# Performance work log

Measured on AMD Instinct MI355X. Metric: run time of the kernel, lower is better.

## Reference

```python
import jax, jax.numpy as jnp
import numpy as np

N_NODES = 50000
N_EDGES = 800000
X_DIM, H_DIM, Y_DIM = 128, 256, 128


def spmm(adj_vals, adj_row, adj_col, x):
    # sparse [N,N] @ dense [N,D] via gather + segment scatter-add
    msgs = adj_vals[:, None] * x[adj_col]  # [E, D]
    return jax.ops.segment_sum(msgs, adj_row, num_segments=N_NODES)


def setup_inputs() -> dict:
    key = jax.random.key(0)
    ks = jax.random.split(key, 6)
    x = jax.random.uniform(ks[0], (N_NODES, X_DIM), dtype=jnp.float32)
    adj_vals = jax.random.uniform(ks[1], (N_EDGES,), dtype=jnp.float32)
    adj_row = jax.random.randint(ks[2], (N_EDGES,), 0, N_NODES, dtype=jnp.int32)
    adj_col = jax.random.randint(ks[3], (N_EDGES,), 0, N_NODES, dtype=jnp.int32)
    W1 = jax.random.normal(ks[4], (X_DIM, H_DIM), dtype=jnp.float32) * (1.0 / np.sqrt(X_DIM))
    b1 = jnp.zeros((H_DIM,), dtype=jnp.float32)
    W2 = jax.random.normal(ks[5], (H_DIM, Y_DIM), dtype=jnp.float32) * (1.0 / np.sqrt(H_DIM))
    b2 = jnp.zeros((Y_DIM,), dtype=jnp.float32)
    return {"x": x, "adj_vals": adj_vals, "adj_row": adj_row, "adj_col": adj_col,
            "W1": W1, "b1": b1, "W2": W2, "b2": b2}


def reference(x, adj_vals, adj_row, adj_col, W1, b1, W2, b2):
    # row-normalize features: x / (sum_j x_ij + 1e-4)
    x = x / (jnp.sum(x, axis=1, keepdims=True) + 1e-4)
    # layer 1: spmm -> linear -> relu (dropout is identity at eval)
    h = jax.nn.relu(spmm(adj_vals, adj_row, adj_col, x) @ W1 + b1)  # [N, H]
    # layer 2: spmm -> linear
    y = spmm(adj_vals, adj_row, adj_col, h) @ W2 + b2  # [N, Y]
    return y
```

## Files before the change

### kernel.cpp

```cpp
#include <hip/hip_runtime.h>

#define N_NODES 50000
#define N_EDGES 800000
#define X_DIM 128
#define H_DIM 256
#define Y_DIM 128

typedef unsigned int uint32;
typedef unsigned short ushort16;
typedef __attribute__((ext_vector_type(8))) short short8;
typedef __attribute__((ext_vector_type(4))) float floatx4;

__device__ inline ushort16 f2bf(float f) {
    uint32 u = __float_as_uint(f);
    return (ushort16)((u + 0x7FFFu + ((u >> 16) & 1u)) >> 16);
}
__device__ inline float bf_lo(uint32 u) { return __uint_as_float(u << 16); }
__device__ inline float bf_hi(uint32 u) { return __uint_as_float(u & 0xFFFF0000u); }

#define BUCKET_SHIFT 7
#define NB 391
#define CHUNK 4096
#define NCHUNK 196
#define CAP_B 2560

#define NORM_BLOCKS 12500
#define CONV_BLOCKS 256

__global__ __launch_bounds__(256) void prep_kernel(
    const float* __restrict__ x, uint32* __restrict__ xb,
    const float* __restrict__ W1, const float* __restrict__ W2,
    ushort16* __restrict__ W1t, ushort16* __restrict__ W2t,
    const int* __restrict__ rows, int* __restrict__ gpartial) {
    int b = blockIdx.x;
    if (b < NORM_BLOCKS) {
        int row = (b * 256 + threadIdx.x) >> 6;
        int lane = threadIdx.x & 63;
        float2 v = ((const float2*)x)[(size_t)row * 64 + lane];
        float s = v.x + v.y;
        #pragma unroll
        for (int off = 32; off > 0; off >>= 1) s += __shfl_xor(s, off, 64);
        float inv = 1.0f / (s + 1e-4f);
        uint32 lo = (uint32)f2bf(v.x * inv);
        uint32 hi = (uint32)f2bf(v.y * inv);
        xb[(size_t)row * 64 + lane] = lo | (hi << 16);
    } else if (b < NORM_BLOCKS + CONV_BLOCKS) {
        int t = (b - NORM_BLOCKS) * 256 + threadIdx.x;
        if (t < X_DIM * H_DIM) {
            int n = t >> 7, k = t & 127;
            W1t[t] = f2bf(W1[k * H_DIM + n]);
        } else {
            int u = t - X_DIM * H_DIM;
            int y = u >> 8, k = u & 255;
            W2t[u] = f2bf(W2[k * Y_DIM + y]);
        }
    } else {
        __shared__ int h[NB];
        int j = b - NORM_BLOCKS - CONV_BLOCKS;
        int t = threadIdx.x;
        for (int i = t; i < NB; i += 256) h[i] = 0;
        __syncthreads();
        int base = j * CHUNK;
        #pragma unroll
        for (int k = 0; k < CHUNK / 256; k++) {
            int e = base + t + k * 256;
            if (e < N_EDGES) atomicAdd(&h[rows[e] >> BUCKET_SHIFT], 1);
        }
        __syncthreads();
        for (int i = t; i < NB; i += 256) gpartial[j * NB + i] = h[i];
    }
}

__global__ __launch_bounds__(512) void bucket_scan_kernel(
    const int* __restrict__ gpartial, int* __restrict__ bucket_base,
    int* __restrict__ bcursor, int* __restrict__ rowptr) {
    __shared__ int s[512];
    int t = threadIdx.x;
    int total = 0;
    if (t < NB) {
        #pragma unroll 4
        for (int j = 0; j < NCHUNK; j++) total += gpartial[j * NB + t];
    }
    s[t] = total;
    __syncthreads();
    #pragma unroll
    for (int off = 1; off < 512; off <<= 1) {
        int u = (t >= off) ? s[t - off] : 0;
        __syncthreads();
        s[t] += u;
        __syncthreads();
    }
    if (t < NB) {
        int excl = s[t] - total;
        bucket_base[t] = excl;
        bcursor[t] = excl;
    }
    if (t == 0) { bucket_base[NB] = N_EDGES; rowptr[N_NODES] = N_EDGES; }
}

__global__ __launch_bounds__(512) void bucketize_kernel(
    const int* __restrict__ rows, const int* __restrict__ cols,
    const float* __restrict__ vals, const int* __restrict__ gpartial,
    int* __restrict__ bcursor, int2* __restrict__ edges) {
    __shared__ int ob[512];
    __shared__ int c[NB];
    __shared__ int g[NB];
    __shared__ int2 buf[CHUNK];
    int t = threadIdx.x;
    int j = blockIdx.x;
    int base = j * CHUNK;
    int M = N_EDGES - base; if (M > CHUNK) M = CHUNK;
    int cnt = (t < NB) ? gpartial[j * NB + t] : 0;
    ob[t] = cnt;
    __syncthreads();
    #pragma unroll
    for (int off = 1; off < 512; off <<= 1) {
        int u = (t >= off) ? ob[t - off] : 0;
        __syncthreads();
        ob[t] += u;
        __syncthreads();
    }
    ob[t] -= cnt;
    if (t < NB) {
        c[t] = 0;
        g[t] = (cnt > 0) ? atomicAdd(&bcursor[t], cnt) : 0;
    }
    __syncthreads();
    #pragma unroll
    for (int k = 0; k < CHUNK / 512; k++) {
        int e = base + t + k * 512;
        if (e < N_EDGES) {
            int r = rows[e];
            int bb = r >> BUCKET_SHIFT;
            int p = ob[bb] + atomicAdd(&c[bb], 1);
            buf[p] = make_int2(cols[e] | ((r & 127) << 16) | (bb << 23),
                               __float_as_int(vals[e]));
        }
    }
    __syncthreads();
    for (int i = t; i < M; i += 512) {
        int2 e = buf[i];
        int bb = (int)((uint32)e.x >> 23);
        edges[g[bb] + (i - ob[bb])] = e;
    }
}

__global__ __launch_bounds__(256) void bucket_sort_kernel(
    const int* __restrict__ bucket_base, int2* __restrict__ edges,
    int2* __restrict__ scratch, int* __restrict__ rowptr) {
    __shared__ int2 buf[CAP_B];
    __shared__ int2 buf2[CAP_B];
    __shared__ int h[128], o[128], c[128];
    int b = blockIdx.x, t = threadIdx.x;
    int base = bucket_base[b];
    int cnt = bucket_base[b + 1] - base;
    bool fits = (cnt <= CAP_B);
    if (t < 128) h[t] = 0;
    __syncthreads();
    for (int i = t; i < cnt; i += 256) {
        int2 e = edges[base + i];
        if (fits) buf[i] = e; else scratch[base + i] = e;
        atomicAdd(&h[(e.x >> 16) & 127], 1);
    }
    __syncthreads();
    int valh = (t < 128) ? h[t] : 0;
    #pragma unroll
    for (int off = 1; off < 128; off <<= 1) {
        int u = (t >= off && t < 128) ? h[t - off] : 0;
        __syncthreads();
        if (t < 128) h[t] += u;
        __syncthreads();
    }
    if (t < 128) {
        o[t] = h[t] - valh;
        c[t] = 0;
        int i = (b << BUCKET_SHIFT) + t;
        if (i < N_NODES) rowptr[i] = base + h[t] - valh;
    }
    __syncthreads();
    for (int i = t; i < cnt; i += 256) {
        int2 e = fits ? buf[i] : scratch[base + i];
        int lr = (e.x >> 16) & 127;
        int p = o[lr] + atomicAdd(&c[lr], 1);
        if (fits) buf2[p] = e; else edges[base + p] = e;
    }
    __syncthreads();
    if (fits)
        for (int i = t; i < cnt; i += 256) edges[base + i] = buf2[i];
}

__device__ inline void spmm_row2(const uint2* __restrict__ feat2,
                                 const int2* __restrict__ edges,
                                 int start, int end, int lane,
                                 float& A0, float& A1, float& A2, float& A3) {
    const int hl = lane & 31;
    const int bsrc = lane & 32;
    float x0 = 0.f, x1 = 0.f, x2 = 0.f, x3 = 0.f;
    int cur = start;
    while (__any(cur < end)) {
        int n = end - cur;
        n = n < 0 ? 0 : (n > 32 ? 32 : n);
        int2 ev = make_int2(0, 0);
        if (hl < n) ev = edges[cur + hl];
        int c = ev.x & 0xFFFF;
        float v = __int_as_float(ev.y);
        int na = __shfl(n, 0, 64), nb = __shfl(n, 32, 64);
        int nm = na > nb ? na : nb;
        int jm = (nm + 7) & ~7;
        for (int j = 0; j < jm; j += 8) {
            int c0 = __shfl(c, bsrc + j, 64),     c1 = __shfl(c, bsrc + j + 1, 64);
            int c2 = __shfl(c, bsrc + j + 2, 64), c3 = __shfl(c, bsrc + j + 3, 64);
            int c4 = __shfl(c, bsrc + j + 4, 64), c5 = __shfl(c, bsrc + j + 5, 64);
            int c6 = __shfl(c, bsrc + j + 6, 64), c7 = __shfl(c, bsrc + j + 7, 64);
            float v0 = __shfl(v, bsrc + j, 64),     v1 = __shfl(v, bsrc + j + 1, 64);
            float v2 = __shfl(v, bsrc + j + 2, 64), v3 = __shfl(v, bsrc + j + 3, 64);
            float v4 = __shfl(v, bsrc + j + 4, 64), v5 = __shfl(v, bsrc + j + 5, 64);
            float v6 = __shfl(v, bsrc + j + 6, 64), v7 = __shfl(v, bsrc + j + 7, 64);
            uint2 f0 = feat2[(size_t)c0 * 32 + hl];
            uint2 f1 = feat2[(size_t)c1 * 32 + hl];
            uint2 f2 = feat2[(size_t)c2 * 32 + hl];
            uint2 f3 = feat2[(size_t)c3 * 32 + hl];
            uint2 f4 = feat2[(size_t)c4 * 32 + hl];
            uint2 f5 = feat2[(size_t)c5 * 32 + hl];
            uint2 f6 = feat2[(size_t)c6 * 32 + hl];
            uint2 f7 = feat2[(size_t)c7 * 32 + hl];
            x0 += v0 * bf_lo(f0.x); x1 += v0 * bf_hi(f0.x);
            x2 += v0 * bf_lo(f0.y); x3 += v0 * bf_hi(f0.y);
            x0 += v1 * bf_lo(f1.x); x1 += v1 * bf_hi(f1.x);
            x2 += v1 * bf_lo(f1.y); x3 += v1 * bf_hi(f1.y);
            x0 += v2 * bf_lo(f2.x); x1 += v2 * bf_hi(f2.x);
            x2 += v2 * bf_lo(f2.y); x3 += v2 * bf_hi(f2.y);
            x0 += v3 * bf_lo(f3.x); x1 += v3 * bf_hi(f3.x);
            x2 += v3 * bf_lo(f3.y); x3 += v3 * bf_hi(f3.y);
            x0 += v4 * bf_lo(f4.x); x1 += v4 * bf_hi(f4.x);
            x2 += v4 * bf_lo(f4.y); x3 += v4 * bf_hi(f4.y);
            x0 += v5 * bf_lo(f5.x); x1 += v5 * bf_hi(f5.x);
            x2 += v5 * bf_lo(f5.y); x3 += v5 * bf_hi(f5.y);
            x0 += v6 * bf_lo(f6.x); x1 += v6 * bf_hi(f6.x);
            x2 += v6 * bf_lo(f6.y); x3 += v6 * bf_hi(f6.y);
            x0 += v7 * bf_lo(f7.x); x1 += v7 * bf_hi(f7.x);
            x2 += v7 * bf_lo(f7.y); x3 += v7 * bf_hi(f7.y);
        }
        cur += n;
    }
    A0 = x0; A1 = x1; A2 = x2; A3 = x3;
}

__global__ __launch_bounds__(512, 4) void spmm_gemm_fused(
    const uint32* __restrict__ xb, const int* __restrict__ rowptr,
    const int2* __restrict__ edges, const ushort16* __restrict__ W1t,
    const ushort16* __restrict__ W2t, const float* __restrict__ b1,
    ushort16* __restrict__ hw) {
    __shared__ ushort16 a_s[64 * 136];
    __shared__ ushort16 h_s[64 * 264];
    const int tx = threadIdx.x;
    const int wave = tx >> 6, lane = tx & 63;
    const int quad = lane >> 4, l16 = lane & 15;
    const int half = lane >> 5, hl = lane & 31;
    const int row0 = blockIdx.x * 64;
    const uint2* xb2 = (const uint2*)xb;

    for (int i = 0; i < 4; i++) {
        int r = wave * 8 + i * 2 + half;
        int row = row0 + r;
        int s = 0, e = 0;
        if (row < N_NODES) { s = rowptr[row]; e = rowptr[row + 1]; }
        float a0, a1, a2, a3;
        spmm_row2(xb2, edges, s, e, lane, a0, a1, a2, a3);
        uint32 lo = (uint32)f2bf(a0) | ((uint32)f2bf(a1) << 16);
        uint32 hi = (uint32)f2bf(a2) | ((uint32)f2bf(a3) << 16);
        *(uint2*)&a_s[r * 136 + hl * 4] = make_uint2(lo, hi);
    }

    short8 bfr1[2][4];
    #pragma unroll
    for (int ct = 0; ct < 2; ct++)
        #pragma unroll
        for (int kk = 0; kk < 4; kk++)
            bfr1[ct][kk] = *(const short8*)
                &W1t[(wave * 32 + ct * 16 + l16) * 128 + kk * 32 + quad * 8];
    __syncthreads();

    floatx4 acc1[4][2];
    #pragma unroll
    for (int rs = 0; rs < 4; rs++)
        #pragma unroll
        for (int ct = 0; ct < 2; ct++)
            #pragma unroll
            for (int j = 0; j < 4; j++) acc1[rs][ct][j] = 0.f;
    #pragma unroll
    for (int kk = 0; kk < 4; kk++) {
        #pragma unroll
        for (int rs = 0; rs < 4; rs++) {
            short8 af = *(const short8*)&a_s[(rs * 16 + l16) * 136 + kk * 32 + quad * 8];
            #pragma unroll
            for (int ct = 0; ct < 2; ct++)
                acc1[rs][ct] = __builtin_amdgcn_mfma_f32_16x16x32_bf16(
                    af, bfr1[ct][kk], acc1[rs][ct], 0, 0, 0);
        }
    }
    float bv[2];
    #pragma unroll
    for (int ct = 0; ct < 2; ct++) bv[ct] = b1[wave * 32 + ct * 16 + l16];
    #pragma unroll
    for (int rs = 0; rs < 4; rs++)
        #pragma unroll
        for (int ct = 0; ct < 2; ct++)
            #pragma unroll
            for (int reg = 0; reg < 4; reg++) {
                float v = acc1[rs][ct][reg] + bv[ct];
                v = v > 0.f ? v : 0.f;
                h_s[(rs * 16 + quad * 4 + reg) * 264 + wave * 32 + ct * 16 + l16] = f2bf(v);
            }

    short8 bfr2[8];
    #pragma unroll
    for (int kk = 0; kk < 8; kk++)
        bfr2[kk] = *(const short8*)
            &W2t[(wave * 16 + l16) * 256 + kk * 32 + quad * 8];
    __syncthreads();

    floatx4 acc2[4];
    #pragma unroll
    for (int rs = 0; rs < 4; rs++)
        #pragma unroll
        for (int j = 0; j < 4; j++) acc2[rs][j] = 0.f;
    #pragma unroll
    for (int kk = 0; kk < 8; kk++) {
        #pragma unroll
        for (int rs = 0; rs < 4; rs++) {
            short8 af = *(const short8*)&h_s[(rs * 16 + l16) * 264 + kk * 32 + quad * 8];
            acc2[rs] = __builtin_amdgcn_mfma_f32_16x16x32_bf16(
                af, bfr2[kk], acc2[rs], 0, 0, 0);
        }
    }
    #pragma unroll
    for (int rs = 0; rs < 4; rs++)
        #pragma unroll
        for (int reg = 0; reg < 4; reg++) {
            int row = row0 + rs * 16 + quad * 4 + reg;
            if (row < N_NODES)
                hw[(size_t)row * 128 + wave * 16 + l16] = f2bf(acc2[rs][reg]);
        }
}

__global__ __launch_bounds__(256) void spmm_out_kernel(
    const uint32* __restrict__ feat, const int* __restrict__ rowptr,
    const int2* __restrict__ edges, const float* __restrict__ bias,
    float* __restrict__ out) {
    int w = (blockIdx.x * blockDim.x + threadIdx.x) >> 6;
    int lane = threadIdx.x & 63;
    int half = lane >> 5, hl = lane & 31;
    int row = w * 2 + half;
    int s = rowptr[row], e = rowptr[row + 1];
    float a0, a1, a2, a3;
    spmm_row2((const uint2*)feat, edges, s, e, lane, a0, a1, a2, a3);
    float4 b = ((const float4*)bias)[hl];
    ((float4*)out)[(size_t)row * 32 + hl] =
        make_float4(a0 + b.x, a1 + b.y, a2 + b.z, a3 + b.w);
}

extern "C" void kernel_launch(void* const* d_in, const int* in_sizes, int n_in,
                              void* d_out, int out_size, void* d_ws, size_t ws_size,
                              hipStream_t stream) {
    const float* x = (const float*)d_in[0];
    const float* adj_vals = (const float*)d_in[1];
    const int* adj_row = (const int*)d_in[2];
    const int* adj_col = (const int*)d_in[3];
    const float* W1 = (const float*)d_in[4];
    const float* b1 = (const float*)d_in[5];
    const float* W2 = (const float*)d_in[6];
    const float* b2 = (const float*)d_in[7];
    float* out = (float*)d_out;

    char* ws = (char*)d_ws;
    uint32*   xb       = (uint32*)  (ws + 0);
    ushort16* hw       = (ushort16*)(ws + 12800000);
    int2*     edges    = (int2*)    (ws + 25600000);
    int2*     scratch  = (int2*)    (ws + 32000000);
    int*      gpartial = (int*)     (ws + 38400000);
    int*      rowptr   = (int*)     (ws + 38713344);
    int*      bbase    = (int*)     (ws + 38914048);
    int*      bcursor  = (int*)     (ws + 38916096);
    ushort16* W1t      = (ushort16*)(ws + 38918144);
    ushort16* W2t      = (ushort16*)(ws + 38983680);

    hipLaunchKernelGGL(prep_kernel, dim3(NORM_BLOCKS + CONV_BLOCKS + NCHUNK),
                       dim3(256), 0, stream, x, xb, W1, W2, W1t, W2t,
                       adj_row, gpartial);

    hipLaunchKernelGGL(bucket_scan_kernel, dim3(1), dim3(512),
                       0, stream, gpartial, bbase, bcursor, rowptr);

    hipLaunchKernelGGL(bucketize_kernel, dim3(NCHUNK), dim3(512),
                       0, stream, adj_row, adj_col, adj_vals, gpartial, bcursor, edges);
    hipLaunchKernelGGL(bucket_sort_kernel, dim3(NB), dim3(256),
                       0, stream, bbase, edges, scratch, rowptr);

    hipLaunchKernelGGL(spmm_gemm_fused, dim3((N_NODES + 63) / 64), dim3(512),
                       0, stream, xb, rowptr, edges, W1t, W2t, b1, hw);

    hipLaunchKernelGGL(spmm_out_kernel, dim3(N_NODES / 8), dim3(256),
                       0, stream, (const uint32*)hw, rowptr, edges, b2, out);
}
```

Measured before the change: 214.1 us.

## Sort edges by column panel within each row for cache-local gathers

The bucket sort now keys each edge on (column panel, local row), splitting columns into four panels, and emits a 4-way segmented row pointer array. Both SpMM kernels walk the panels in an outer loop so every wave in the GPU gathers feature rows from the same quarter of the table at once, which should improve L2 locality. Other changes: edges are read with nontemporal loads, outputs are written with nontemporal stores, the gather unroll drops from 8 to 4, occupancy hints rise to 6, and spmm_out is resized to 64-row blocks of 512 threads. In exchange there are four times as many segment loops per row and a larger scan in the sort kernel.

```diff
diff --git a/kernel.cpp b/kernel.cpp
--- a/kernel.cpp
+++ b/kernel.cpp
@@ -23,6 +23,11 @@
 #define CHUNK 4096
 #define NCHUNK 196
 #define CAP_B 2560
+
+#define PS 12512
+__device__ inline int panel_of(int col) {
+    return (col >= 2 * PS) ? ((col >= 3 * PS) ? 3 : 2) : ((col >= PS) ? 1 : 0);
+}
 
 #define NORM_BLOCKS 12500
 #define CONV_BLOCKS 256
@@ -73,7 +78,7 @@
 
 __global__ __launch_bounds__(512) void bucket_scan_kernel(
     const int* __restrict__ gpartial, int* __restrict__ bucket_base,
-    int* __restrict__ bcursor, int* __restrict__ rowptr) {
+    int* __restrict__ bcursor, int* __restrict__ rp4) {
     __shared__ int s[512];
     int t = threadIdx.x;
     int total = 0;
@@ -95,7 +100,7 @@
         bucket_base[t] = excl;
         bcursor[t] = excl;
     }
-    if (t == 0) { bucket_base[NB] = N_EDGES; rowptr[N_NODES] = N_EDGES; }
+    if (t == 0) { bucket_base[NB] = N_EDGES; rp4[NB * 512] = N_EDGES; }
 }
 
 __global__ __launch_bounds__(512) void bucketize_kernel(
@@ -145,109 +150,94 @@
     }
 }
 
-__global__ __launch_bounds__(256) void bucket_sort_kernel(
+__global__ __launch_bounds__(512) void bucket_sort_kernel(
     const int* __restrict__ bucket_base, int2* __restrict__ edges,
-    int2* __restrict__ scratch, int* __restrict__ rowptr) {
+    int2* __restrict__ scratch, int* __restrict__ rp4) {
     __shared__ int2 buf[CAP_B];
     __shared__ int2 buf2[CAP_B];
-    __shared__ int h[128], o[128], c[128];
+    __shared__ int h[512], o[512], c[512];
     int b = blockIdx.x, t = threadIdx.x;
     int base = bucket_base[b];
     int cnt = bucket_base[b + 1] - base;
     bool fits = (cnt <= CAP_B);
-    if (t < 128) h[t] = 0;
-    __syncthreads();
-    for (int i = t; i < cnt; i += 256) {
+    h[t] = 0;
+    __syncthreads();
+    for (int i = t; i < cnt; i += 512) {
         int2 e = edges[base + i];
         if (fits) buf[i] = e; else scratch[base + i] = e;
-        atomicAdd(&h[(e.x >> 16) & 127], 1);
-    }
-    __syncthreads();
-    int valh = (t < 128) ? h[t] : 0;
-    #pragma unroll
-    for (int off = 1; off < 128; off <<= 1) {
-        int u = (t >= off && t < 128) ? h[t - off] : 0;
-        __syncthreads();
-        if (t < 128) h[t] += u;
-        __syncthreads();
-    }
-    if (t < 128) {
-        o[t] = h[t] - valh;
-        c[t] = 0;
-        int i = (b << BUCKET_SHIFT) + t;
-        if (i < N_NODES) rowptr[i] = base + h[t] - valh;
-    }
-    __syncthreads();
-    for (int i = t; i < cnt; i += 256) {
+        int col = e.x & 0xFFFF;
+        int key = (panel_of(col) << 7) + ((e.x >> 16) & 127);
+        atomicAdd(&h[key], 1);
+    }
+    __syncthreads();
+    int valh = h[t];
+    #pragma unroll
+    for (int off = 1; off < 512; off <<= 1) {
+        int u = (t >= off) ? h[t - off] : 0;
+        __syncthreads();
+        h[t] += u;
+        __syncthreads();
+    }
+    int excl = h[t] - valh;
+    o[t] = excl;
+    c[t] = 0;
+    rp4[(b << 9) + t] = base + excl;
+    __syncthreads();
+    for (int i = t; i < cnt; i += 512) {
         int2 e = fits ? buf[i] : scratch[base + i];
-        int lr = (e.x >> 16) & 127;
-        int p = o[lr] + atomicAdd(&c[lr], 1);
+        int col = e.x & 0xFFFF;
+        int key = (panel_of(col) << 7) + ((e.x >> 16) & 127);
+        int p = o[key] + atomicAdd(&c[key], 1);
         if (fits) buf2[p] = e; else edges[base + p] = e;
     }
     __syncthreads();
     if (fits)
-        for (int i = t; i < cnt; i += 256) edges[base + i] = buf2[i];
-}
-
-__device__ inline void spmm_row2(const uint2* __restrict__ feat2,
-                                 const int2* __restrict__ edges,
-                                 int start, int end, int lane,
-                                 float& A0, float& A1, float& A2, float& A3) {
+        for (int i = t; i < cnt; i += 512) edges[base + i] = buf2[i];
+}
+
+__device__ __forceinline__ void spmm_seg2(const uint2* __restrict__ feat2,
+                                          const int2* __restrict__ edges,
+                                          int start, int end, int lane,
+                                          float& A0, float& A1, float& A2, float& A3) {
     const int hl = lane & 31;
     const int bsrc = lane & 32;
-    float x0 = 0.f, x1 = 0.f, x2 = 0.f, x3 = 0.f;
     int cur = start;
     while (__any(cur < end)) {
         int n = end - cur;
         n = n < 0 ? 0 : (n > 32 ? 32 : n);
-        int2 ev = make_int2(0, 0);
-        if (hl < n) ev = edges[cur + hl];
-        int c = ev.x & 0xFFFF;
-        float v = __int_as_float(ev.y);
+        unsigned long long evu = 0;
+        if (hl < n)
+            evu = __builtin_nontemporal_load(
+                (const unsigned long long*)(edges + cur + hl));
+        int c = (int)(evu & 0xFFFFull);
+        float v = __uint_as_float((uint32)(evu >> 32));
         int na = __shfl(n, 0, 64), nb = __shfl(n, 32, 64);
         int nm = na > nb ? na : nb;
-        int jm = (nm + 7) & ~7;
-        for (int j = 0; j < jm; j += 8) {
+        int jm = (nm + 3) & ~3;
+        for (int j = 0; j < jm; j += 4) {
             int c0 = __shfl(c, bsrc + j, 64),     c1 = __shfl(c, bsrc + j + 1, 64);
             int c2 = __shfl(c, bsrc + j + 2, 64), c3 = __shfl(c, bsrc + j + 3, 64);
-            int c4 = __shfl(c, bsrc + j + 4, 64), c5 = __shfl(c, bsrc + j + 5, 64);
-            int c6 = __shfl(c, bsrc + j + 6, 64), c7 = __shfl(c, bsrc + j + 7, 64);
             float v0 = __shfl(v, bsrc + j, 64),     v1 = __shfl(v, bsrc + j + 1, 64);
             float v2 = __shfl(v, bsrc + j + 2, 64), v3 = __shfl(v, bsrc + j + 3, 64);
-            float v4 = __shfl(v, bsrc + j + 4, 64), v5 = __shfl(v, bsrc + j + 5, 64);
-            float v6 = __shfl(v, bsrc + j + 6, 64), v7 = __shfl(v, bsrc + j + 7, 64);
             uint2 f0 = feat2[(size_t)c0 * 32 + hl];
             uint2 f1 = feat2[(size_t)c1 * 32 + hl];
             uint2 f2 = feat2[(size_t)c2 * 32 + hl];
             uint2 f3 = feat2[(size_t)c3 * 32 + hl];
-            uint2 f4 = feat2[(size_t)c4 * 32 + hl];
-            uint2 f5 = feat2[(size_t)c5 * 32 + hl];
-            uint2 f6 = feat2[(size_t)c6 * 32 + hl];
-            uint2 f7 = feat2[(size_t)c7 * 32 + hl];
-            x0 += v0 * bf_lo(f0.x); x1 += v0 * bf_hi(f0.x);
-            x2 += v0 * bf_lo(f0.y); x3 += v0 * bf_hi(f0.y);
-            x0 += v1 * bf_lo(f1.x); x1 += v1 * bf_hi(f1.x);
-            x2 += v1 * bf_lo(f1.y); x3 += v1 * bf_hi(f1.y);
-            x0 += v2 * bf_lo(f2.x); x1 += v2 * bf_hi(f2.x);
-            x2 += v2 * bf_lo(f2.y); x3 += v2 * bf_hi(f2.y);
-            x0 += v3 * bf_lo(f3.x); x1 += v3 * bf_hi(f3.x);
-            x2 += v3 * bf_lo(f3.y); x3 += v3 * bf_hi(f3.y);
-            x0 += v4 * bf_lo(f4.x); x1 += v4 * bf_hi(f4.x);
-            x2 += v4 * bf_lo(f4.y); x3 += v4 * bf_hi(f4.y);
-            x0 += v5 * bf_lo(f5.x); x1 += v5 * bf_hi(f5.x);
-            x2 += v5 * bf_lo(f5.y); x3 += v5 * bf_hi(f5.y);
-            x0 += v6 * bf_lo(f6.x); x1 += v6 * bf_hi(f6.x);
-            x2 += v6 * bf_lo(f6.y); x3 += v6 * bf_hi(f6.y);
-            x0 += v7 * bf_lo(f7.x); x1 += v7 * bf_hi(f7.x);
-            x2 += v7 * bf_lo(f7.y); x3 += v7 * bf_hi(f7.y);
+            A0 += v0 * bf_lo(f0.x); A1 += v0 * bf_hi(f0.x);
+            A2 += v0 * bf_lo(f0.y); A3 += v0 * bf_hi(f0.y);
+            A0 += v1 * bf_lo(f1.x); A1 += v1 * bf_hi(f1.x);
+            A2 += v1 * bf_lo(f1.y); A3 += v1 * bf_hi(f1.y);
+            A0 += v2 * bf_lo(f2.x); A1 += v2 * bf_hi(f2.x);
+            A2 += v2 * bf_lo(f2.y); A3 += v2 * bf_hi(f2.y);
+            A0 += v3 * bf_lo(f3.x); A1 += v3 * bf_hi(f3.x);
+            A2 += v3 * bf_lo(f3.y); A3 += v3 * bf_hi(f3.y);
         }
         cur += n;
     }
-    A0 = x0; A1 = x1; A2 = x2; A3 = x3;
-}
-
-__global__ __launch_bounds__(512, 4) void spmm_gemm_fused(
-    const uint32* __restrict__ xb, const int* __restrict__ rowptr,
+}
+
+__global__ __launch_bounds__(512, 6) void spmm_gemm_fused(
+    const uint32* __restrict__ xb, const int* __restrict__ rp4,
     const int2* __restrict__ edges, const ushort16* __restrict__ W1t,
     const ushort16* __restrict__ W2t, const float* __restrict__ b1,
     ushort16* __restrict__ hw) {
@@ -258,17 +248,32 @@
     const int quad = lane >> 4, l16 = lane & 15;
     const int half = lane >> 5, hl = lane & 31;
     const int row0 = blockIdx.x * 64;
+    const int bkt = row0 >> 7;
     const uint2* xb2 = (const uint2*)xb;
 
+    float ac[4][4];
+    #pragma unroll
+    for (int i = 0; i < 4; i++)
+        #pragma unroll
+        for (int d = 0; d < 4; d++) ac[i][d] = 0.f;
+    for (int p = 0; p < 4; p++) {
+        #pragma unroll
+        for (int i = 0; i < 4; i++) {
+            int row = row0 + wave * 8 + i * 2 + half;
+            int s = 0, e = 0;
+            if (row < N_NODES) {
+                int idx = (bkt << 9) + (p << 7) + (row & 127);
+                s = rp4[idx];
+                e = rp4[idx + 1];
+            }
+            spmm_seg2(xb2, edges, s, e, lane, ac[i][0], ac[i][1], ac[i][2], ac[i][3]);
+        }
+    }
+    #pragma unroll
     for (int i = 0; i < 4; i++) {
         int r = wave * 8 + i * 2 + half;
-        int row = row0 + r;
-        int s = 0, e = 0;
-        if (row < N_NODES) { s = rowptr[row]; e = rowptr[row + 1]; }
-        float a0, a1, a2, a3;
-        spmm_row2(xb2, edges, s, e, lane, a0, a1, a2, a3);
-        uint32 lo = (uint32)f2bf(a0) | ((uint32)f2bf(a1) << 16);
-        uint32 hi = (uint32)f2bf(a2) | ((uint32)f2bf(a3) << 16);
+        uint32 lo = (uint32)f2bf(ac[i][0]) | ((uint32)f2bf(ac[i][1]) << 16);
+        uint32 hi = (uint32)f2bf(ac[i][2]) | ((uint32)f2bf(ac[i][3]) << 16);
         *(uint2*)&a_s[r * 136 + hl * 4] = make_uint2(lo, hi);
     }
 
@@ -340,24 +345,54 @@
         for (int reg = 0; reg < 4; reg++) {
             int row = row0 + rs * 16 + quad * 4 + reg;
             if (row < N_NODES)
-                hw[(size_t)row * 128 + wave * 16 + l16] = f2bf(acc2[rs][reg]);
-        }
-}
-
-__global__ __launch_bounds__(256) void spmm_out_kernel(
-    const uint32* __restrict__ feat, const int* __restrict__ rowptr,
+                __builtin_nontemporal_store(
+                    f2bf(acc2[rs][reg]),
+                    &hw[(size_t)row * 128 + wave * 16 + l16]);
+        }
+}
+
+__global__ __launch_bounds__(512, 6) void spmm_out_kernel(
+    const uint32* __restrict__ feat, const int* __restrict__ rp4,
     const int2* __restrict__ edges, const float* __restrict__ bias,
     float* __restrict__ out) {
-    int w = (blockIdx.x * blockDim.x + threadIdx.x) >> 6;
-    int lane = threadIdx.x & 63;
-    int half = lane >> 5, hl = lane & 31;
-    int row = w * 2 + half;
-    int s = rowptr[row], e = rowptr[row + 1];
-    float a0, a1, a2, a3;
-    spmm_row2((const uint2*)feat, edges, s, e, lane, a0, a1, a2, a3);
-    float4 b = ((const float4*)bias)[hl];
-    ((float4*)out)[(size_t)row * 32 + hl] =
-        make_float4(a0 + b.x, a1 + b.y, a2 + b.z, a3 + b.w);
+    const int tx = threadIdx.x;
+    const int wave = tx >> 6, lane = tx & 63;
+    const int half = lane >> 5, hl = lane & 31;
+    const int row0 = blockIdx.x * 64;
+    const int bkt = row0 >> 7;
+    const uint2* f2 = (const uint2*)feat;
+
+    float ac[4][4];
+    #pragma unroll
+    for (int i = 0; i < 4; i++)
+        #pragma unroll
+        for (int d = 0; d < 4; d++) ac[i][d] = 0.f;
+    for (int p = 0; p < 4; p++) {
+        #pragma unroll
+        for (int i = 0; i < 4; i++) {
+            int row = row0 + wave * 8 + i * 2 + half;
+            int s = 0, e = 0;
+            if (row < N_NODES) {
+                int idx = (bkt << 9) + (p << 7) + (row & 127);
+                s = rp4[idx];
+                e = rp4[idx + 1];
+            }
+            spmm_seg2(f2, edges, s, e, lane, ac[i][0], ac[i][1], ac[i][2], ac[i][3]);
+        }
+    }
+    float4 bv = ((const float4*)bias)[hl];
+    #pragma unroll
+    for (int i = 0; i < 4; i++) {
+        int row = row0 + wave * 8 + i * 2 + half;
+        if (row < N_NODES) {
+            floatx4 o4;
+            o4[0] = ac[i][0] + bv.x;
+            o4[1] = ac[i][1] + bv.y;
+            o4[2] = ac[i][2] + bv.z;
+            o4[3] = ac[i][3] + bv.w;
+            __builtin_nontemporal_store(o4, (floatx4*)out + (size_t)row * 32 + hl);
+        }
+    }
 }
 
 extern "C" void kernel_launch(void* const* d_in, const int* in_sizes, int n_in,
@@ -379,27 +414,27 @@
     int2*     edges    = (int2*)    (ws + 25600000);
     int2*     scratch  = (int2*)    (ws + 32000000);
     int*      gpartial = (int*)     (ws + 38400000);
-    int*      rowptr   = (int*)     (ws + 38713344);
-    int*      bbase    = (int*)     (ws + 38914048);
-    int*      bcursor  = (int*)     (ws + 38916096);
-    ushort16* W1t      = (ushort16*)(ws + 38918144);
-    ushort16* W2t      = (ushort16*)(ws + 38983680);
+    int*      rp4      = (int*)     (ws + 38707200);
+    int*      bbase    = (int*)     (ws + 39508480);
+    int*      bcursor  = (int*)     (ws + 39510528);
+    ushort16* W1t      = (ushort16*)(ws + 39512576);
+    ushort16* W2t      = (ushort16*)(ws + 39578112);
 
     hipLaunchKernelGGL(prep_kernel, dim3(NORM_BLOCKS + CONV_BLOCKS + NCHUNK),
                        dim3(256), 0, stream, x, xb, W1, W2, W1t, W2t,
                        adj_row, gpartial);
 
     hipLaunchKernelGGL(bucket_scan_kernel, dim3(1), dim3(512),
-                       0, stream, gpartial, bbase, bcursor, rowptr);
+                       0, stream, gpartial, bbase, bcursor, rp4);
 
     hipLaunchKernelGGL(bucketize_kernel, dim3(NCHUNK), dim3(512),
                        0, stream, adj_row, adj_col, adj_vals, gpartial, bcursor, edges);
-    hipLaunchKernelGGL(bucket_sort_kernel, dim3(NB), dim3(256),
-                       0, stream, bbase, edges, scratch, rowptr);
+    hipLaunchKernelGGL(bucket_sort_kernel, dim3(NB), dim3(512),
+                       0, stream, bbase, edges, scratch, rp4);
 
     hipLaunchKernelGGL(spmm_gemm_fused, dim3((N_NODES + 63) / 64), dim3(512),
-                       0, stream, xb, rowptr, edges, W1t, W2t, b1, hw);
-
-    hipLaunchKernelGGL(spmm_out_kernel, dim3(N_NODES / 8), dim3(256),
-                       0, stream, (const uint32*)hw, rowptr, edges, b2, out);
-}
+                       0, stream, xb, rp4, edges, W1t, W2t, b1, hw);
+
+    hipLaunchKernelGGL(spmm_out_kernel, dim3((N_NODES + 63) / 64), dim3(512),
+                       0, stream, (const uint32*)hw, rp4, edges, b2, out);
+}
```

Measured after the change: 254.3 us. 1.19x slower.
